# Performance work log

Hardware: AMD Instinct MI355X
Metric: run time of the kernel (lower is better)

## Reference

```python
import jax, jax.numpy as jnp
import numpy as np

N_ATOMS = 8192
N_PAIRS = 65536
F = 128        # n_atombasis
R = 20         # n_radialbasis
B = 5          # graph_n_blocks
EPS = 1e-8     # stability constant


def setup_inputs() -> dict:
    key = jax.random.key(0)
    ks = jax.random.split(key, 16)
    rn = lambda k, shape, s=0.05: jax.random.normal(k, shape, dtype=jnp.float32) * s
    return {
        "features": jax.random.normal(ks[0], (N_ATOMS, F), jnp.float32),
        "distances": jax.random.uniform(ks[1], (N_PAIRS,), jnp.float32, 0.5, 5.0),
        "vectors": jax.random.normal(ks[2], (N_PAIRS, 3), jnp.float32),
        "cutoffs": jax.random.uniform(ks[3], (N_PAIRS,), jnp.float32),
        "rbfs": jax.random.normal(ks[4], (N_PAIRS, R), jnp.float32),
        "filter_W": rn(ks[5], (R, B * 3 * F)),
        "filter_b": jnp.zeros((B * 3 * F,), jnp.float32),
        "int_W1": rn(ks[6], (B, F, F)),
        "int_b1": jnp.zeros((B, F), jnp.float32),
        "int_W2": rn(ks[7], (B, F, 3 * F)),
        "int_b2": jnp.zeros((B, 3 * F), jnp.float32),
        "mix_Wv": rn(ks[8], (B, F, 2 * F)),
        "mix_W1": rn(ks[9], (B, 2 * F, F)),
        "mix_b1": jnp.zeros((B, F), jnp.float32),
        "mix_W2": rn(ks[10], (B, F, 3 * F)),
        "mix_b2": jnp.zeros((B, 3 * F), jnp.float32),
        "idx_i": jax.random.randint(ks[11], (N_PAIRS,), 0, N_ATOMS),
        "idx_j": jax.random.randint(ks[12], (N_PAIRS,), 0, N_ATOMS),
    }


def reference(features, distances, vectors, cutoffs, rbfs,
              filter_W, filter_b, int_W1, int_b1, int_W2, int_b2,
              mix_Wv, mix_W1, mix_b1, mix_W2, mix_b2, idx_i, idx_j):
    n_atoms = features.shape[0]
    # Cutoff-weighted radial filters, one (3F) chunk per block: [P, B*3F]
    descriptors = (rbfs @ filter_W + filter_b) * cutoffs[:, None]
    dir_ij = vectors / distances[:, None]                       # [P, 3]

    q = features[:, None, :]                                    # [N, 1, F]
    mu = jnp.zeros((n_atoms, 3, F), dtype=features.dtype)       # [N, 3, F]

    for b in range(B):
        # --- interaction block ---
        x = jax.nn.silu(q @ int_W1[b] + int_b1[b]) @ int_W2[b] + int_b2[b]  # [N,1,3F]
        Wij = descriptors[:, None, b * 3 * F:(b + 1) * 3 * F]               # [P,1,3F]
        xj = x[idx_j] * Wij                                                 # [P,1,3F]
        muj = mu[idx_j]                                                     # [P,3,F]
        dq, dmuR, dmumu = jnp.split(xj, 3, axis=-1)                         # [P,1,F] each
        dmu = dmuR * dir_ij[:, :, None] + dmumu * muj                       # [P,3,F]
        q = q + jax.ops.segment_sum(dq, idx_i, num_segments=n_atoms)
        mu = mu + jax.ops.segment_sum(dmu, idx_i, num_segments=n_atoms)

        # --- mixing block ---
        mu_V, mu_W = jnp.split(mu @ mix_Wv[b], 2, axis=-1)                  # [N,3,F] each
        mu_Vn = jnp.sqrt(jnp.sum(mu_V ** 2, axis=-2, keepdims=True) + EPS)  # [N,1,F]
        ctx = jnp.concatenate([q, mu_Vn], axis=-1)                          # [N,1,2F]
        y = jax.nn.silu(ctx @ mix_W1[b] + mix_b1[b]) @ mix_W2[b] + mix_b2[b]
        dq_i, dmu_i, dqmu_i = jnp.split(y, 3, axis=-1)                      # [N,1,F] each
        q = q + dq_i + dqmu_i * jnp.sum(mu_V * mu_W, axis=1, keepdims=True)
        mu = mu + dmu_i * mu_W

    return q[:, 0, :], mu
```

## Files before the change

### kernel.cpp

```cpp
#include <hip/hip_runtime.h>
#include <hip/hip_bf16.h>

#define NA 8192
#define NP 65536
#define WROW 1920
#define CAP 40

typedef short short8 __attribute__((ext_vector_type(8)));
typedef short short4v __attribute__((ext_vector_type(4)));
typedef float floatx4 __attribute__((ext_vector_type(4)));
typedef unsigned uint3v __attribute__((ext_vector_type(3)));

static __device__ __forceinline__ short f2bf(float f) {
    union { float f; unsigned u; } v; v.f = f;
    unsigned r = v.u + 0x7FFF + ((v.u >> 16) & 1);
    return (short)(r >> 16);
}
static __device__ __forceinline__ float bf2f(short s) {
    union { unsigned u; float f; } v;
    v.u = ((unsigned)(unsigned short)s) << 16;
    return v.f;
}
static __device__ __forceinline__ unsigned char f2fp8(float f) {
    int p = __builtin_amdgcn_cvt_pk_fp8_f32(f, 0.f, 0, false);
    return (unsigned char)(p & 0xFF);
}
static __device__ __forceinline__ float fp82f(unsigned char b) {
    return __builtin_amdgcn_cvt_f32_fp8((int)b, 0);
}
static __device__ __forceinline__ float silu(float v) {
    return v / (1.f + __expf(-v));
}

static __device__ __forceinline__ void swz(const float* __restrict__ src,
                                           short* __restrict__ dst,
                                           int K, int N, int idx) {
    int kn = K * N;
    int b = idx / kn;
    int r = idx - b * kn;
    int tile = r >> 9, li = r & 511;
    int lane = li >> 3, bb = li & 7;
    int Kt = K >> 5;
    int nt = tile / Kt, kt = tile - nt * Kt;
    int k = kt * 32 + (lane >> 4) * 8 + bb;
    int n = nt * 16 + (lane & 15);
    dst[idx] = f2bf(src[b * kn + k * N + n]);
}

__global__ __launch_bounds__(256) void k_setup(const float* __restrict__ iW1,
                                               const float* __restrict__ iW2,
                                               const float* __restrict__ mWv,
                                               const float* __restrict__ mW1,
                                               const float* __restrict__ mW2,
                                               const float* __restrict__ fW,
                                               short* __restrict__ W1t,
                                               short* __restrict__ W2t,
                                               short* __restrict__ Wvt,
                                               short* __restrict__ mW1t,
                                               short* __restrict__ mW2t,
                                               short* __restrict__ fWt,
                                               const float* __restrict__ feat,
                                               float* __restrict__ q,
                                               float* __restrict__ mu,
                                               short* __restrict__ q_bf,
                                               unsigned* __restrict__ xmu_u,
                                               int* __restrict__ cursor) {
    int idx = blockIdx.x * 256 + threadIdx.x;
    if (idx < 962560) {
        if (idx < 81920)       { swz(iW1, W1t, 128, 128, idx); return; }
        idx -= 81920;
        if (idx < 245760)      { swz(iW2, W2t, 128, 384, idx); return; }
        idx -= 245760;
        if (idx < 163840)      { swz(mWv, Wvt, 128, 256, idx); return; }
        idx -= 163840;
        if (idx < 163840)      { swz(mW1, mW1t, 256, 128, idx); return; }
        idx -= 163840;
        if (idx < 245760)      { swz(mW2, mW2t, 128, 384, idx); return; }
        idx -= 245760;
        {
            int b = idx / 12288;
            int r = idx - b * 12288;
            int nt = r >> 9;
            int li = r & 511;
            int lane = li >> 3, bb = li & 7;
            int k = (lane >> 4) * 8 + bb;
            int n = nt * 16 + (lane & 15);
            fWt[b * 12288 + r] = (k < 20) ? f2bf(fW[k * WROW + b * 384 + n]) : (short)0;
        }
        return;
    }
    idx -= 962560;
    if (idx < NA * 128) { float v = feat[idx]; q[idx] = v; q_bf[idx] = f2bf(v); }
    mu[idx] = 0.f;
    xmu_u[idx] = 0;
    if (idx < NA) cursor[idx] = 0;
}

__global__ __launch_bounds__(256) void k_fillprep(const int* __restrict__ idx_i,
                                                  const int* __restrict__ idx_j,
                                                  int* __restrict__ cursor,
                                                  const float* __restrict__ cut,
                                                  const float* __restrict__ dist,
                                                  const float* __restrict__ vec,
                                                  const float* __restrict__ rbfs,
                                                  float* __restrict__ cut_csr,
                                                  float4* __restrict__ dirj,
                                                  short* __restrict__ rbf_c) {
    int p = blockIdx.x * 256 + threadIdx.x;
    if (p >= NP) return;
    int i = idx_i[p];
    int pos = atomicAdd(&cursor[i], 1);
    if (pos >= CAP) return;
    int e = i * CAP + pos;
    float c = cut[p];
    cut_csr[e] = c;
    float invd = 1.f / dist[p];
    float4 d;
    d.x = vec[p * 3 + 0] * invd;
    d.y = vec[p * 3 + 1] * invd;
    d.z = vec[p * 3 + 2] * invd;
    d.w = __int_as_float(idx_j[p]);
    dirj[e] = d;
    #pragma unroll
    for (int k = 0; k < 20; ++k) rbf_c[e * 32 + k] = f2bf(rbfs[p * 20 + k] * c);
    #pragma unroll
    for (int k = 20; k < 32; ++k) rbf_c[e * 32 + k] = 0;
}

__global__ __launch_bounds__(256) void k_x(const short* __restrict__ q_bf,
                                           const short* __restrict__ W1sw,
                                           const short* __restrict__ W2sw,
                                           const float* __restrict__ b1,
                                           const float* __restrict__ b2,
                                           unsigned char* __restrict__ xmu) {
    __shared__ __align__(16) short qtile[16 * 136];
    __shared__ __align__(16) short hs[16 * 136];
    int t = threadIdx.x;
    int wv = t >> 6, lane = t & 63, quad = lane >> 4, l16 = lane & 15;
    int a0 = blockIdx.x * 16;

    #pragma unroll
    for (int it = 0; it < 2; ++it) {
        int c = it * 256 + t;
        int row = c >> 5, col4 = c & 31;
        *(short4v*)(qtile + row * 136 + col4 * 4) =
            *(const short4v*)(q_bf + (a0 + row) * 128 + col4 * 4);
    }
    __syncthreads();

    floatx4 acc0 = {0.f, 0.f, 0.f, 0.f}, acc1 = {0.f, 0.f, 0.f, 0.f};
    #pragma unroll
    for (int kk = 0; kk < 4; ++kk) {
        short8 a  = *(const short8*)(qtile + l16 * 136 + kk * 32 + quad * 8);
        short8 b0 = *(const short8*)(W1sw + ((wv * 2 + 0) * 4 + kk) * 512 + lane * 8);
        short8 bq = *(const short8*)(W1sw + ((wv * 2 + 1) * 4 + kk) * 512 + lane * 8);
        acc0 = __builtin_amdgcn_mfma_f32_16x16x32_bf16(a, b0, acc0, 0, 0, 0);
        acc1 = __builtin_amdgcn_mfma_f32_16x16x32_bf16(a, bq, acc1, 0, 0, 0);
    }
    __syncthreads();
    {
        int n0 = wv * 32 + l16;
        float bia0 = b1[n0], bia1 = b1[n0 + 16];
        #pragma unroll
        for (int r = 0; r < 4; ++r) {
            int m = quad * 4 + r;
            hs[m * 136 + n0]      = f2bf(silu(acc0[r] + bia0));
            hs[m * 136 + n0 + 16] = f2bf(silu(acc1[r] + bia1));
        }
    }
    __syncthreads();
    floatx4 acc[6];
    #pragma unroll
    for (int jj = 0; jj < 6; ++jj) acc[jj] = {0.f, 0.f, 0.f, 0.f};
    #pragma unroll
    for (int kk = 0; kk < 4; ++kk) {
        short8 a = *(const short8*)(hs + l16 * 136 + kk * 32 + quad * 8);
        #pragma unroll
        for (int jj = 0; jj < 6; ++jj) {
            short8 b = *(const short8*)(W2sw + ((wv * 6 + jj) * 4 + kk) * 512 + lane * 8);
            acc[jj] = __builtin_amdgcn_mfma_f32_16x16x32_bf16(a, b, acc[jj], 0, 0, 0);
        }
    }
    #pragma unroll
    for (int jj = 0; jj < 6; ++jj) {
        int n = wv * 96 + jj * 16 + l16;
        float bia = b2[n];
        #pragma unroll
        for (int r = 0; r < 4; ++r) {
            int m = quad * 4 + r;
            xmu[(size_t)((a0 + m) * 128 + (n & 127)) * 12 + (n >> 7)] =
                f2fp8(acc[jj][r] + bia);
        }
    }
}

__global__ __launch_bounds__(256, 4) void k_gather(const unsigned char* __restrict__ xmu,
                                                   const short* __restrict__ rbf_c,
                                                   const short* __restrict__ fWt,
                                                   const float* __restrict__ fbp,
                                                   const float4* __restrict__ dirj,
                                                   const float* __restrict__ cut_csr,
                                                   const int* __restrict__ cursor,
                                                   short* __restrict__ dqg,
                                                   short* __restrict__ dmug) {
    __shared__ short dlds[16 * 392];
    __shared__ float pm[3 * 512];
    int i = blockIdx.x;
    int t = threadIdx.x;
    int wv = t >> 6, lane = t & 63, quad = lane >> 4, l16 = lane & 15;
    int start = i * CAP;

    float4 dj[4];
    #pragma unroll
    for (int m = 0; m < 4; ++m) dj[m] = dirj[start + wv + 4 * m];
    short8 afrag = *(const short8*)(rbf_c + (start + l16) * 32 + quad * 8);
    float cc[4];
    #pragma unroll
    for (int r = 0; r < 4; ++r) cc[r] = cut_csr[start + quad * 4 + r];

    int cnt = cursor[i];
    if (cnt > CAP) cnt = CAP;
    int end = start + cnt;

    float acc[8];
    #pragma unroll
    for (int k = 0; k < 8; ++k) acc[k] = 0.f;

    for (int e0 = start; e0 < end; e0 += 16) {
        if (e0 > start) {
            __syncthreads();
            #pragma unroll
            for (int m = 0; m < 4; ++m) dj[m] = dirj[e0 + wv + 4 * m];
            afrag = *(const short8*)(rbf_c + (e0 + l16) * 32 + quad * 8);
            #pragma unroll
            for (int r = 0; r < 4; ++r) cc[r] = cut_csr[e0 + quad * 4 + r];
        }
        int clen = end - e0; if (clen > 16) clen = 16;
        #pragma unroll
        for (int nt = 0; nt < 6; ++nt) {
            int col = wv * 96 + nt * 16 + l16;
            short8 bfr = *(const short8*)(fWt + (wv * 6 + nt) * 512 + lane * 8);
            floatx4 z = {0.f, 0.f, 0.f, 0.f};
            floatx4 ad = __builtin_amdgcn_mfma_f32_16x16x32_bf16(afrag, bfr, z, 0, 0, 0);
            float fbv = fbp[col];
            dlds[(quad * 4 + 0) * 392 + col] = f2bf(ad[0] + fbv * cc[0]);
            dlds[(quad * 4 + 1) * 392 + col] = f2bf(ad[1] + fbv * cc[1]);
            dlds[(quad * 4 + 2) * 392 + col] = f2bf(ad[2] + fbv * cc[2]);
            dlds[(quad * 4 + 3) * 392 + col] = f2bf(ad[3] + fbv * cc[3]);
        }
        uint3v rl[4], rh[4];
        #pragma unroll
        for (int m = 0; m < 4; ++m) {
            int le = wv + 4 * m;
            int j = (le < clen) ? __float_as_int(dj[m].w) : 0;
            const unsigned char* base = xmu + (size_t)j * 1536 + lane * 12;
            rl[m] = *(const uint3v*)(base);
            rh[m] = *(const uint3v*)(base + 768);
        }
        __syncthreads();
        #pragma unroll
        for (int m = 0; m < 4; ++m) {
            int le = wv + 4 * m;
            if (le < clen) {
                float wa0 = bf2f(dlds[le * 392 + lane]);
                float wb0 = bf2f(dlds[le * 392 + 128 + lane]);
                float wc0 = bf2f(dlds[le * 392 + 256 + lane]);
                float wa1 = bf2f(dlds[le * 392 + 64 + lane]);
                float wb1 = bf2f(dlds[le * 392 + 192 + lane]);
                float wc1 = bf2f(dlds[le * 392 + 320 + lane]);
                {
                    uint3v r_ = rl[m];
                    float x0 = fp82f((unsigned char)(r_.x & 0xFF));
                    float x1 = fp82f((unsigned char)((r_.x >> 8) & 0xFF));
                    float x2 = fp82f((unsigned char)((r_.x >> 16) & 0xFF));
                    float u0 = bf2f((short)(r_.y & 0xFFFF));
                    float u1 = bf2f((short)(r_.y >> 16));
                    float u2 = bf2f((short)(r_.z & 0xFFFF));
                    acc[0] += x0 * wa0;
                    float xb = x1 * wb0, xc = x2 * wc0;
                    acc[1] += xb * dj[m].x + xc * u0;
                    acc[2] += xb * dj[m].y + xc * u1;
                    acc[3] += xb * dj[m].z + xc * u2;
                }
                {
                    uint3v r_ = rh[m];
                    float x0 = fp82f((unsigned char)(r_.x & 0xFF));
                    float x1 = fp82f((unsigned char)((r_.x >> 8) & 0xFF));
                    float x2 = fp82f((unsigned char)((r_.x >> 16) & 0xFF));
                    float u0 = bf2f((short)(r_.y & 0xFFFF));
                    float u1 = bf2f((short)(r_.y >> 16));
                    float u2 = bf2f((short)(r_.z & 0xFFFF));
                    acc[4] += x0 * wa1;
                    float xb = x1 * wb1, xc = x2 * wc1;
                    acc[5] += xb * dj[m].x + xc * u0;
                    acc[6] += xb * dj[m].y + xc * u1;
                    acc[7] += xb * dj[m].z + xc * u2;
                }
            }
        }
    }
    if (wv) {
        float* p = pm + (wv - 1) * 512;
        #pragma unroll
        for (int arr = 0; arr < 4; ++arr) {
            p[arr * 128 + lane]      = acc[arr];
            p[arr * 128 + 64 + lane] = acc[arr + 4];
        }
    }
    __syncthreads();
    if (wv == 0) {
        #pragma unroll
        for (int hi = 0; hi < 2; ++hi) {
            int f = lane + hi * 64;
            float s[4];
            #pragma unroll
            for (int arr = 0; arr < 4; ++arr)
                s[arr] = acc[arr + 4 * hi]
                       + pm[0 * 512 + arr * 128 + f]
                       + pm[1 * 512 + arr * 128 + f]
                       + pm[2 * 512 + arr * 128 + f];
            dqg[i * 128 + f]            = f2bf(s[0]);
            dmug[(i * 3 + 0) * 128 + f] = f2bf(s[1]);
            dmug[(i * 3 + 1) * 128 + f] = f2bf(s[2]);
            dmug[(i * 3 + 2) * 128 + f] = f2bf(s[3]);
        }
    }
}

__global__ __launch_bounds__(512, 4) void k_mixx(const float* __restrict__ mu_ro,
                                                 const short* __restrict__ dmug,
                                                 const float* __restrict__ q_ro,
                                                 const short* __restrict__ dqg,
                                                 const short* __restrict__ Wvsw,
                                                 const short* __restrict__ W1sw,
                                                 const short* __restrict__ W2sw,
                                                 const float* __restrict__ b1,
                                                 const float* __restrict__ b2,
                                                 float* __restrict__ q,
                                                 float* __restrict__ mu,
                                                 unsigned char* __restrict__ xmu,
                                                 const short* __restrict__ xW1sw,
                                                 const short* __restrict__ xW2sw,
                                                 const float* __restrict__ xb1,
                                                 const float* __restrict__ xb2,
                                                 int do_x) {
    __shared__ __align__(16) char smem[51968];
    short* ms    = (short*)(smem);
    short* qtile = (short*)(smem + 13056);
    short* Vv    = (short*)(smem + 17408);
    short* hs    = (short*)(smem + 17408);
    short* Vw    = (short*)(smem + 30464);
    short* vnb   = (short*)(smem + 43520);
    short* sb    = (short*)(smem + 47872);
    int t = threadIdx.x;
    int wv = t >> 6, lane = t & 63, quad = lane >> 4, l16 = lane & 15;
    int a0 = blockIdx.x * 16;
    int co = wv * 16 + l16;

    float qnf[4];
    float mnf[4][3];
    #pragma unroll
    for (int r = 0; r < 4; ++r) {
        int m = quad * 4 + r;
        int ga = a0 + m;
        int gq = ga * 128 + co;
        qnf[r] = q_ro[gq] + bf2f(dqg[gq]);
        qtile[m * 136 + co] = f2bf(qnf[r]);
        #pragma unroll
        for (int d = 0; d < 3; ++d) {
            int gm = (ga * 3 + d) * 128 + co;
            mnf[r][d] = mu_ro[gm] + bf2f(dmug[gm]);
            ms[(m * 3 + d) * 136 + co] = f2bf(mnf[r][d]);
        }
    }
    __syncthreads();

    {
        floatx4 acc[3][2];
        #pragma unroll
        for (int mt = 0; mt < 3; ++mt)
            #pragma unroll
            for (int nt = 0; nt < 2; ++nt) acc[mt][nt] = {0.f, 0.f, 0.f, 0.f};
        #pragma unroll
        for (int kk = 0; kk < 4; ++kk) {
            short8 a[3];
            #pragma unroll
            for (int mt = 0; mt < 3; ++mt)
                a[mt] = *(const short8*)(ms + (mt * 16 + l16) * 136 + kk * 32 + quad * 8);
            #pragma unroll
            for (int nt = 0; nt < 2; ++nt) {
                short8 b = *(const short8*)(Wvsw + ((wv * 2 + nt) * 4 + kk) * 512 + lane * 8);
                #pragma unroll
                for (int mt = 0; mt < 3; ++mt)
                    acc[mt][nt] = __builtin_amdgcn_mfma_f32_16x16x32_bf16(a[mt], b, acc[mt][nt], 0, 0, 0);
            }
        }
        #pragma unroll
        for (int mt = 0; mt < 3; ++mt)
            #pragma unroll
            for (int nt = 0; nt < 2; ++nt)
                #pragma unroll
                for (int r = 0; r < 4; ++r) {
                    int row = mt * 16 + quad * 4 + r;
                    int col = wv * 32 + nt * 16 + l16;
                    short v = f2bf(acc[mt][nt][r]);
                    if (col < 128) Vv[row * 136 + col] = v;
                    else           Vw[row * 136 + col - 128] = v;
                }
    }
    __syncthreads();
    #pragma unroll
    for (int k = 0; k < 4; ++k) {
        int idx = k * 512 + t;
        int a = idx >> 7, c = idx & 127;
        float v0 = bf2f(Vv[(a * 3 + 0) * 136 + c]);
        float v1 = bf2f(Vv[(a * 3 + 1) * 136 + c]);
        float v2 = bf2f(Vv[(a * 3 + 2) * 136 + c]);
        float w0 = bf2f(Vw[(a * 3 + 0) * 136 + c]);
        float w1 = bf2f(Vw[(a * 3 + 1) * 136 + c]);
        float w2 = bf2f(Vw[(a * 3 + 2) * 136 + c]);
        vnb[a * 136 + c] = f2bf(sqrtf(v0 * v0 + v1 * v1 + v2 * v2 + 1e-8f));
        sb[a * 128 + c]  = f2bf(v0 * w0 + v1 * w1 + v2 * w2);
    }
    __syncthreads();
    {
        floatx4 acc0 = {0.f, 0.f, 0.f, 0.f};
        #pragma unroll
        for (int kk = 0; kk < 8; ++kk) {
            short8 a;
            if (kk < 4)
                a = *(const short8*)(qtile + l16 * 136 + kk * 32 + quad * 8);
            else
                a = *(const short8*)(vnb + l16 * 136 + (kk - 4) * 32 + quad * 8);
            short8 b0 = *(const short8*)(W1sw + (wv * 8 + kk) * 512 + lane * 8);
            acc0 = __builtin_amdgcn_mfma_f32_16x16x32_bf16(a, b0, acc0, 0, 0, 0);
        }
        int n0 = wv * 16 + l16;
        float bia0 = b1[n0];
        #pragma unroll
        for (int r = 0; r < 4; ++r) {
            int m = quad * 4 + r;
            hs[m * 136 + n0] = f2bf(silu(acc0[r] + bia0));
        }
    }
    __syncthreads();
    {
        floatx4 accB[3];
        #pragma unroll
        for (int c = 0; c < 3; ++c) accB[c] = {0.f, 0.f, 0.f, 0.f};
        #pragma unroll
        for (int kk = 0; kk < 4; ++kk) {
            short8 a = *(const short8*)(hs + l16 * 136 + kk * 32 + quad * 8);
            #pragma unroll
            for (int c = 0; c < 3; ++c) {
                short8 b = *(const short8*)(W2sw + ((c * 8 + wv) * 4 + kk) * 512 + lane * 8);
                accB[c] = __builtin_amdgcn_mfma_f32_16x16x32_bf16(a, b, accB[c], 0, 0, 0);
            }
        }
        float bq_  = b2[co];
        float bm_  = b2[128 + co];
        float bqm_ = b2[256 + co];
        #pragma unroll
        for (int r = 0; r < 4; ++r) {
            int m = quad * 4 + r;
            int ga = a0 + m;
            float dq   = accB[0][r] + bq_;
            float dmu  = accB[1][r] + bm_;
            float dqmu = accB[2][r] + bqm_;
            float sv = bf2f(sb[m * 128 + co]);
            int gq = ga * 128 + co;
            float qn = qnf[r] + dq + dqmu * sv;
            q[gq] = qn;
            qtile[m * 136 + co] = f2bf(qn);
            float mn[3];
            #pragma unroll
            for (int d = 0; d < 3; ++d) {
                int gm = (ga * 3 + d) * 128 + co;
                float mw = bf2f(Vw[(m * 3 + d) * 136 + co]);
                mn[d] = mnf[r][d] + dmu * mw;
                mu[gm] = mn[d];
            }
            unsigned lo = (unsigned)(unsigned short)f2bf(mn[0]) |
                          ((unsigned)(unsigned short)f2bf(mn[1]) << 16);
            *(unsigned*)(xmu + (size_t)gq * 12 + 4) = lo;
            *(short*)(xmu + (size_t)gq * 12 + 8) = f2bf(mn[2]);
        }
    }
    if (!do_x) return;
    __syncthreads();
    {
        floatx4 acc0 = {0.f, 0.f, 0.f, 0.f};
        #pragma unroll
        for (int kk = 0; kk < 4; ++kk) {
            short8 a  = *(const short8*)(qtile + l16 * 136 + kk * 32 + quad * 8);
            short8 b0 = *(const short8*)(xW1sw + (wv * 4 + kk) * 512 + lane * 8);
            acc0 = __builtin_amdgcn_mfma_f32_16x16x32_bf16(a, b0, acc0, 0, 0, 0);
        }
        int n0 = wv * 16 + l16;
        float bia0 = xb1[n0];
        #pragma unroll
        for (int r = 0; r < 4; ++r) {
            int m = quad * 4 + r;
            hs[m * 136 + n0] = f2bf(silu(acc0[r] + bia0));
        }
    }
    __syncthreads();
    {
        floatx4 acc[3];
        #pragma unroll
        for (int jj = 0; jj < 3; ++jj) acc[jj] = {0.f, 0.f, 0.f, 0.f};
        #pragma unroll
        for (int kk = 0; kk < 4; ++kk) {
            short8 a = *(const short8*)(hs + l16 * 136 + kk * 32 + quad * 8);
            #pragma unroll
            for (int jj = 0; jj < 3; ++jj) {
                short8 b = *(const short8*)(xW2sw + ((wv * 3 + jj) * 4 + kk) * 512 + lane * 8);
                acc[jj] = __builtin_amdgcn_mfma_f32_16x16x32_bf16(a, b, acc[jj], 0, 0, 0);
            }
        }
        #pragma unroll
        for (int jj = 0; jj < 3; ++jj) {
            int n = wv * 48 + jj * 16 + l16;
            float bia = xb2[n];
            #pragma unroll
            for (int r = 0; r < 4; ++r) {
                int m = quad * 4 + r;
                xmu[(size_t)((a0 + m) * 128 + (n & 127)) * 12 + (n >> 7)] =
                    f2fp8(acc[jj][r] + bia);
            }
        }
    }
}

extern "C" void kernel_launch(void* const* d_in, const int* in_sizes, int n_in,
                              void* d_out, int out_size, void* d_ws, size_t ws_size,
                              hipStream_t stream) {
    const float* feat = (const float*)d_in[0];
    const float* dist = (const float*)d_in[1];
    const float* vec  = (const float*)d_in[2];
    const float* cut  = (const float*)d_in[3];
    const float* rbfs = (const float*)d_in[4];
    const float* fW   = (const float*)d_in[5];
    const float* fb   = (const float*)d_in[6];
    const float* iW1  = (const float*)d_in[7];
    const float* ib1  = (const float*)d_in[8];
    const float* iW2  = (const float*)d_in[9];
    const float* ib2  = (const float*)d_in[10];
    const float* mWv  = (const float*)d_in[11];
    const float* mW1  = (const float*)d_in[12];
    const float* mb1  = (const float*)d_in[13];
    const float* mW2  = (const float*)d_in[14];
    const float* mb2  = (const float*)d_in[15];
    const int* idx_i  = (const int*)d_in[16];
    const int* idx_j  = (const int*)d_in[17];

    float* q  = (float*)d_out;
    float* mu = (float*)d_out + NA * 128;

    char* w = (char*)d_ws;
    unsigned char* xmu = (unsigned char*)(w);
    short* dqg     = (short*)(w + 12582912);
    short* q_bf    = (short*)(w + 14680064);
    short* dmug    = (short*)(w + 16777216);
    short* W1t     = (short*)(w + 23068672);
    short* W2t     = (short*)(w + 23232512);
    short* Wvt     = (short*)(w + 23724032);
    short* mW1t    = (short*)(w + 24051712);
    short* mW2t    = (short*)(w + 24379392);
    short* fWt     = (short*)(w + 24870912);
    int*   cursor  = (int*)(w + 24993792);
    float4* dirj   = (float4*)(w + 25026560);
    float* cut_csr = (float*)(w + 30269696);
    short* rbf_c   = (short*)(w + 31580480);

    k_setup<<<16048, 256, 0, stream>>>(iW1, iW2, mWv, mW1, mW2, fW,
                                       W1t, W2t, Wvt, mW1t, mW2t, fWt,
                                       feat, q, mu, q_bf, (unsigned*)xmu, cursor);
    k_fillprep<<<NP / 256, 256, 0, stream>>>(idx_i, idx_j, cursor, cut, dist, vec,
                                             rbfs, cut_csr, dirj, rbf_c);

    k_x<<<NA / 16, 256, 0, stream>>>(q_bf, W1t, W2t, ib1, ib2, xmu);
    for (int b = 0; b < 5; ++b) {
        int bn = (b + 1) % 5;
        k_gather<<<NA, 256, 0, stream>>>(xmu, rbf_c, fWt + b * 12288,
                                         fb + b * 384, dirj, cut_csr, cursor,
                                         dqg, dmug);
        k_mixx<<<NA / 16, 512, 0, stream>>>(mu, dmug, q, dqg,
                                            Wvt + b * 32768,
                                            mW1t + b * 32768, mW2t + b * 49152,
                                            mb1 + b * 128, mb2 + b * 384,
                                            q, mu, xmu,
                                            W1t + bn * 16384, W2t + bn * 49152,
                                            ib1 + bn * 128, ib2 + bn * 384,
                                            (b < 4) ? 1 : 0);
    }
}
```

Baseline: 371.3 us.

## Fuse per-atom gather into mixing kernel with double-buffered xmu

```diff
diff --git a/kernel.cpp b/kernel.cpp
--- a/kernel.cpp
+++ b/kernel.cpp
@@ -194,143 +194,15 @@
     }
 }
 
-__global__ __launch_bounds__(256, 4) void k_gather(const unsigned char* __restrict__ xmu,
-                                                   const short* __restrict__ rbf_c,
-                                                   const short* __restrict__ fWt,
-                                                   const float* __restrict__ fbp,
-                                                   const float4* __restrict__ dirj,
-                                                   const float* __restrict__ cut_csr,
-                                                   const int* __restrict__ cursor,
-                                                   short* __restrict__ dqg,
-                                                   short* __restrict__ dmug) {
-    __shared__ short dlds[16 * 392];
-    __shared__ float pm[3 * 512];
-    int i = blockIdx.x;
-    int t = threadIdx.x;
-    int wv = t >> 6, lane = t & 63, quad = lane >> 4, l16 = lane & 15;
-    int start = i * CAP;
-
-    float4 dj[4];
-    #pragma unroll
-    for (int m = 0; m < 4; ++m) dj[m] = dirj[start + wv + 4 * m];
-    short8 afrag = *(const short8*)(rbf_c + (start + l16) * 32 + quad * 8);
-    float cc[4];
-    #pragma unroll
-    for (int r = 0; r < 4; ++r) cc[r] = cut_csr[start + quad * 4 + r];
-
-    int cnt = cursor[i];
-    if (cnt > CAP) cnt = CAP;
-    int end = start + cnt;
-
-    float acc[8];
-    #pragma unroll
-    for (int k = 0; k < 8; ++k) acc[k] = 0.f;
-
-    for (int e0 = start; e0 < end; e0 += 16) {
-        if (e0 > start) {
-            __syncthreads();
-            #pragma unroll
-            for (int m = 0; m < 4; ++m) dj[m] = dirj[e0 + wv + 4 * m];
-            afrag = *(const short8*)(rbf_c + (e0 + l16) * 32 + quad * 8);
-            #pragma unroll
-            for (int r = 0; r < 4; ++r) cc[r] = cut_csr[e0 + quad * 4 + r];
-        }
-        int clen = end - e0; if (clen > 16) clen = 16;
-        #pragma unroll
-        for (int nt = 0; nt < 6; ++nt) {
-            int col = wv * 96 + nt * 16 + l16;
-            short8 bfr = *(const short8*)(fWt + (wv * 6 + nt) * 512 + lane * 8);
-            floatx4 z = {0.f, 0.f, 0.f, 0.f};
-            floatx4 ad = __builtin_amdgcn_mfma_f32_16x16x32_bf16(afrag, bfr, z, 0, 0, 0);
-            float fbv = fbp[col];
-            dlds[(quad * 4 + 0) * 392 + col] = f2bf(ad[0] + fbv * cc[0]);
-            dlds[(quad * 4 + 1) * 392 + col] = f2bf(ad[1] + fbv * cc[1]);
-            dlds[(quad * 4 + 2) * 392 + col] = f2bf(ad[2] + fbv * cc[2]);
-            dlds[(quad * 4 + 3) * 392 + col] = f2bf(ad[3] + fbv * cc[3]);
-        }
-        uint3v rl[4], rh[4];
-        #pragma unroll
-        for (int m = 0; m < 4; ++m) {
-            int le = wv + 4 * m;
-            int j = (le < clen) ? __float_as_int(dj[m].w) : 0;
-            const unsigned char* base = xmu + (size_t)j * 1536 + lane * 12;
-            rl[m] = *(const uint3v*)(base);
-            rh[m] = *(const uint3v*)(base + 768);
-        }
-        __syncthreads();
-        #pragma unroll
-        for (int m = 0; m < 4; ++m) {
-            int le = wv + 4 * m;
-            if (le < clen) {
-                float wa0 = bf2f(dlds[le * 392 + lane]);
-                float wb0 = bf2f(dlds[le * 392 + 128 + lane]);
-                float wc0 = bf2f(dlds[le * 392 + 256 + lane]);
-                float wa1 = bf2f(dlds[le * 392 + 64 + lane]);
-                float wb1 = bf2f(dlds[le * 392 + 192 + lane]);
-                float wc1 = bf2f(dlds[le * 392 + 320 + lane]);
-                {
-                    uint3v r_ = rl[m];
-                    float x0 = fp82f((unsigned char)(r_.x & 0xFF));
-                    float x1 = fp82f((unsigned char)((r_.x >> 8) & 0xFF));
-                    float x2 = fp82f((unsigned char)((r_.x >> 16) & 0xFF));
-                    float u0 = bf2f((short)(r_.y & 0xFFFF));
-                    float u1 = bf2f((short)(r_.y >> 16));
-                    float u2 = bf2f((short)(r_.z & 0xFFFF));
-                    acc[0] += x0 * wa0;
-                    float xb = x1 * wb0, xc = x2 * wc0;
-                    acc[1] += xb * dj[m].x + xc * u0;
-                    acc[2] += xb * dj[m].y + xc * u1;
-                    acc[3] += xb * dj[m].z + xc * u2;
-                }
-                {
-                    uint3v r_ = rh[m];
-                    float x0 = fp82f((unsigned char)(r_.x & 0xFF));
-                    float x1 = fp82f((unsigned char)((r_.x >> 8) & 0xFF));
-                    float x2 = fp82f((unsigned char)((r_.x >> 16) & 0xFF));
-                    float u0 = bf2f((short)(r_.y & 0xFFFF));
-                    float u1 = bf2f((short)(r_.y >> 16));
-                    float u2 = bf2f((short)(r_.z & 0xFFFF));
-                    acc[4] += x0 * wa1;
-                    float xb = x1 * wb1, xc = x2 * wc1;
-                    acc[5] += xb * dj[m].x + xc * u0;
-                    acc[6] += xb * dj[m].y + xc * u1;
-                    acc[7] += xb * dj[m].z + xc * u2;
-                }
-            }
-        }
-    }
-    if (wv) {
-        float* p = pm + (wv - 1) * 512;
-        #pragma unroll
-        for (int arr = 0; arr < 4; ++arr) {
-            p[arr * 128 + lane]      = acc[arr];
-            p[arr * 128 + 64 + lane] = acc[arr + 4];
-        }
-    }
-    __syncthreads();
-    if (wv == 0) {
-        #pragma unroll
-        for (int hi = 0; hi < 2; ++hi) {
-            int f = lane + hi * 64;
-            float s[4];
-            #pragma unroll
-            for (int arr = 0; arr < 4; ++arr)
-                s[arr] = acc[arr + 4 * hi]
-                       + pm[0 * 512 + arr * 128 + f]
-                       + pm[1 * 512 + arr * 128 + f]
-                       + pm[2 * 512 + arr * 128 + f];
-            dqg[i * 128 + f]            = f2bf(s[0]);
-            dmug[(i * 3 + 0) * 128 + f] = f2bf(s[1]);
-            dmug[(i * 3 + 1) * 128 + f] = f2bf(s[2]);
-            dmug[(i * 3 + 2) * 128 + f] = f2bf(s[3]);
-        }
-    }
-}
-
-__global__ __launch_bounds__(512, 4) void k_mixx(const float* __restrict__ mu_ro,
-                                                 const short* __restrict__ dmug,
+__global__ __launch_bounds__(512, 4) void k_gmix(const unsigned char* __restrict__ xmu_r,
+                                                 const short* __restrict__ rbf_c,
+                                                 const short* __restrict__ fWt,
+                                                 const float* __restrict__ fbp,
+                                                 const float4* __restrict__ dirj,
+                                                 const float* __restrict__ cut_csr,
+                                                 const int* __restrict__ cursor,
+                                                 const float* __restrict__ mu_ro,
                                                  const float* __restrict__ q_ro,
-                                                 const short* __restrict__ dqg,
                                                  const short* __restrict__ Wvsw,
                                                  const short* __restrict__ W1sw,
                                                  const short* __restrict__ W2sw,
@@ -338,23 +210,124 @@
                                                  const float* __restrict__ b2,
                                                  float* __restrict__ q,
                                                  float* __restrict__ mu,
-                                                 unsigned char* __restrict__ xmu,
+                                                 unsigned char* __restrict__ xmu_w,
                                                  const short* __restrict__ xW1sw,
                                                  const short* __restrict__ xW2sw,
                                                  const float* __restrict__ xb1,
                                                  const float* __restrict__ xb2,
                                                  int do_x) {
-    __shared__ __align__(16) char smem[51968];
-    short* ms    = (short*)(smem);
-    short* qtile = (short*)(smem + 13056);
-    short* Vv    = (short*)(smem + 17408);
-    short* hs    = (short*)(smem + 17408);
-    short* Vw    = (short*)(smem + 30464);
-    short* vnb   = (short*)(smem + 43520);
-    short* sb    = (short*)(smem + 47872);
+    __shared__ __align__(16) char smem[68608];
+    short* dg = (short*)smem;
     int t = threadIdx.x;
     int wv = t >> 6, lane = t & 63, quad = lane >> 4, l16 = lane & 15;
     int a0 = blockIdx.x * 16;
+
+    {
+        short* dld = (short*)(smem + 16640 + wv * 6272);
+        #pragma unroll
+        for (int half = 0; half < 2; ++half) {
+            int la = wv + half * 8;
+            int i  = __builtin_amdgcn_readfirstlane(a0 + la);
+            int start = i * CAP;
+            int cnt = cursor[i];
+            if (cnt > CAP) cnt = CAP;
+            float acc[8];
+            #pragma unroll
+            for (int k = 0; k < 8; ++k) acc[k] = 0.f;
+            for (int e0 = start; e0 < start + cnt; e0 += 8) {
+                int clen = start + cnt - e0; if (clen > 8) clen = 8;
+                short8 afrag = *(const short8*)(rbf_c + (size_t)(e0 + l16) * 32 + quad * 8);
+                float cc[4];
+                #pragma unroll
+                for (int r = 0; r < 4; ++r)
+                    cc[r] = cut_csr[e0 + (quad & 1) * 4 + r];
+                #pragma unroll
+                for (int nt = 0; nt < 24; ++nt) {
+                    short8 bfr = *(const short8*)(fWt + nt * 512 + lane * 8);
+                    floatx4 z = {0.f, 0.f, 0.f, 0.f};
+                    floatx4 ad = __builtin_amdgcn_mfma_f32_16x16x32_bf16(afrag, bfr, z, 0, 0, 0);
+                    if (quad < 2) {
+                        int col = nt * 16 + l16;
+                        float fbv = fbp[col];
+                        #pragma unroll
+                        for (int r = 0; r < 4; ++r)
+                            dld[(quad * 4 + r) * 392 + col] = f2bf(ad[r] + fbv * cc[r]);
+                    }
+                }
+                #pragma unroll
+                for (int mb = 0; mb < 8; mb += 4) {
+                    int mcl = clen - mb;
+                    if (mcl > 0) {
+                        float4 dj[4]; uint3v rl[4], rh[4];
+                        #pragma unroll
+                        for (int m = 0; m < 4; ++m)
+                            if (m < mcl) dj[m] = dirj[e0 + mb + m];
+                        #pragma unroll
+                        for (int m = 0; m < 4; ++m)
+                            if (m < mcl) {
+                                const unsigned char* base =
+                                    xmu_r + (size_t)__float_as_int(dj[m].w) * 1536 + lane * 12;
+                                rl[m] = *(const uint3v*)(base);
+                                rh[m] = *(const uint3v*)(base + 768);
+                            }
+                        #pragma unroll
+                        for (int m = 0; m < 4; ++m)
+                            if (m < mcl) {
+                                int le = mb + m;
+                                float wa0 = bf2f(dld[le * 392 + lane]);
+                                float wb0 = bf2f(dld[le * 392 + 128 + lane]);
+                                float wc0 = bf2f(dld[le * 392 + 256 + lane]);
+                                float wa1 = bf2f(dld[le * 392 + 64 + lane]);
+                                float wb1 = bf2f(dld[le * 392 + 192 + lane]);
+                                float wc1 = bf2f(dld[le * 392 + 320 + lane]);
+                                {
+                                    uint3v r_ = rl[m];
+                                    float x0 = fp82f((unsigned char)(r_.x & 0xFF));
+                                    float x1 = fp82f((unsigned char)((r_.x >> 8) & 0xFF));
+                                    float x2 = fp82f((unsigned char)((r_.x >> 16) & 0xFF));
+                                    float u0 = bf2f((short)(r_.y & 0xFFFF));
+                                    float u1 = bf2f((short)(r_.y >> 16));
+                                    float u2 = bf2f((short)(r_.z & 0xFFFF));
+                                    acc[0] += x0 * wa0;
+                                    float xb = x1 * wb0, xc = x2 * wc0;
+                                    acc[1] += xb * dj[m].x + xc * u0;
+                                    acc[2] += xb * dj[m].y + xc * u1;
+                                    acc[3] += xb * dj[m].z + xc * u2;
+                                }
+                                {
+                                    uint3v r_ = rh[m];
+                                    float x0 = fp82f((unsigned char)(r_.x & 0xFF));
+                                    float x1 = fp82f((unsigned char)((r_.x >> 8) & 0xFF));
+                                    float x2 = fp82f((unsigned char)((r_.x >> 16) & 0xFF));
+                                    float u0 = bf2f((short)(r_.y & 0xFFFF));
+                                    float u1 = bf2f((short)(r_.y >> 16));
+                                    float u2 = bf2f((short)(r_.z & 0xFFFF));
+                                    acc[4] += x0 * wa1;
+                                    float xb = x1 * wb1, xc = x2 * wc1;
+                                    acc[5] += xb * dj[m].x + xc * u0;
+                                    acc[6] += xb * dj[m].y + xc * u1;
+                                    acc[7] += xb * dj[m].z + xc * u2;
+                                }
+                            }
+                    }
+                }
+            }
+            #pragma unroll
+            for (int arr = 0; arr < 4; ++arr) {
+                dg[(la * 4 + arr) * 130 + lane]      = f2bf(acc[arr]);
+                dg[(la * 4 + arr) * 130 + 64 + lane] = f2bf(acc[arr + 4]);
+            }
+        }
+    }
+    __syncthreads();
+
+    short* ms    = (short*)(smem + 16640);
+    short* qtile = (short*)(smem + 16640 + 13056);
+    short* Vv    = (short*)(smem + 16640 + 17408);
+    short* hs    = (short*)(smem + 16640 + 17408);
+    short* Vw    = (short*)(smem + 16640 + 30464);
+    short* vnb   = (short*)(smem + 16640 + 43520);
+    short* sb    = (short*)(smem + 16640 + 47872);
     int co = wv * 16 + l16;
 
     float qnf[4];
@@ -364,12 +337,12 @@
         int m = quad * 4 + r;
         int ga = a0 + m;
         int gq = ga * 128 + co;
-        qnf[r] = q_ro[gq] + bf2f(dqg[gq]);
+        qnf[r] = q_ro[gq] + bf2f(dg[(m * 4 + 0) * 130 + co]);
         qtile[m * 136 + co] = f2bf(qnf[r]);
         #pragma unroll
         for (int d = 0; d < 3; ++d) {
             int gm = (ga * 3 + d) * 128 + co;
-            mnf[r][d] = mu_ro[gm] + bf2f(dmug[gm]);
+            mnf[r][d] = mu_ro[gm] + bf2f(dg[(m * 4 + 1 + d) * 130 + co]);
             ms[(m * 3 + d) * 136 + co] = f2bf(mnf[r][d]);
         }
     }
@@ -482,8 +455,8 @@
             }
             unsigned lo = (unsigned)(unsigned short)f2bf(mn[0]) |
                           ((unsigned)(unsigned short)f2bf(mn[1]) << 16);
-            *(unsigned*)(xmu + (size_t)gq * 12 + 4) = lo;
-            *(short*)(xmu + (size_t)gq * 12 + 8) = f2bf(mn[2]);
+            *(unsigned*)(xmu_w + (size_t)gq * 12 + 4) = lo;
+            *(short*)(xmu_w + (size_t)gq * 12 + 8) = f2bf(mn[2]);
         }
     }
     if (!do_x) return;
@@ -525,7 +498,7 @@
             #pragma unroll
             for (int r = 0; r < 4; ++r) {
                 int m = quad * 4 + r;
-                xmu[(size_t)((a0 + m) * 128 + (n & 127)) * 12 + (n >> 7)] =
+                xmu_w[(size_t)((a0 + m) * 128 + (n & 127)) * 12 + (n >> 7)] =
                     f2fp8(acc[jj][r] + bia);
             }
         }
@@ -558,38 +531,37 @@
     float* mu = (float*)d_out + NA * 128;
 
     char* w = (char*)d_ws;
-    unsigned char* xmu = (unsigned char*)(w);
-    short* dqg     = (short*)(w + 12582912);
-    short* q_bf    = (short*)(w + 14680064);
-    short* dmug    = (short*)(w + 16777216);
-    short* W1t     = (short*)(w + 23068672);
-    short* W2t     = (short*)(w + 23232512);
-    short* Wvt     = (short*)(w + 23724032);
-    short* mW1t    = (short*)(w + 24051712);
-    short* mW2t    = (short*)(w + 24379392);
-    short* fWt     = (short*)(w + 24870912);
-    int*   cursor  = (int*)(w + 24993792);
-    float4* dirj   = (float4*)(w + 25026560);
-    float* cut_csr = (float*)(w + 30269696);
-    short* rbf_c   = (short*)(w + 31580480);
+    unsigned char* xmu0 = (unsigned char*)(w);
+    unsigned char* xmu1 = (unsigned char*)(w + 12582912);
+    short* q_bf    = (short*)(w + 25165824);
+    short* W1t     = (short*)(w + 27262976);
+    short* W2t     = (short*)(w + 27426816);
+    short* Wvt     = (short*)(w + 27918336);
+    short* mW1t    = (short*)(w + 28246016);
+    short* mW2t    = (short*)(w + 28573696);
+    short* fWt     = (short*)(w + 29065216);
+    int*   cursor  = (int*)(w + 29188096);
+    float4* dirj   = (float4*)(w + 29220864);
+    float* cut_csr = (float*)(w + 34464000);
+    short* rbf_c   = (short*)(w + 35774784);
 
     k_setup<<<16048, 256, 0, stream>>>(iW1, iW2, mWv, mW1, mW2, fW,
                                        W1t, W2t, Wvt, mW1t, mW2t, fWt,
-                                       feat, q, mu, q_bf, (unsigned*)xmu, cursor);
+                                       feat, q, mu, q_bf, (unsigned*)xmu0, cursor);
     k_fillprep<<<NP / 256, 256, 0, stream>>>(idx_i, idx_j, cursor, cut, dist, vec,
                                              rbfs, cut_csr, dirj, rbf_c);
 
-    k_x<<<NA / 16, 256, 0, stream>>>(q_bf, W1t, W2t, ib1, ib2, xmu);
+    k_x<<<NA / 16, 256, 0, stream>>>(q_bf, W1t, W2t, ib1, ib2, xmu0);
+    unsigned char* xb[2] = {xmu0, xmu1};
     for (int b = 0; b < 5; ++b) {
         int bn = (b + 1) % 5;
-        k_gather<<<NA, 256, 0, stream>>>(xmu, rbf_c, fWt + b * 12288,
-                                         fb + b * 384, dirj, cut_csr, cursor,
-                                         dqg, dmug);
-        k_mixx<<<NA / 16, 512, 0, stream>>>(mu, dmug, q, dqg,
+        k_gmix<<<NA / 16, 512, 0, stream>>>(xb[b & 1], rbf_c, fWt + b * 12288,
+                                            fb + b * 384, dirj, cut_csr, cursor,
+                                            mu, q,
                                             Wvt + b * 32768,
                                             mW1t + b * 32768, mW2t + b * 49152,
                                             mb1 + b * 128, mb2 + b * 384,
-                                            q, mu, xmu,
+                                            q, mu, xb[(b + 1) & 1],
                                             W1t + bn * 16384, W2t + bn * 49152,
                                             ib1 + bn * 128, ib2 + bn * 384,
                                             (b < 4) ? 1 : 0);
```

Measured after the change: 498.1 us. 1.34x slower.

## Split packed x/mu gather array into separate double-buffered x and mu arrays

Applied to the files above, without the earlier changes.

```diff
diff --git a/kernel.cpp b/kernel.cpp
--- a/kernel.cpp
+++ b/kernel.cpp
@@ -9,7 +9,6 @@
 typedef short short8 __attribute__((ext_vector_type(8)));
 typedef short short4v __attribute__((ext_vector_type(4)));
 typedef float floatx4 __attribute__((ext_vector_type(4)));
-typedef unsigned uint3v __attribute__((ext_vector_type(3)));
 
 static __device__ __forceinline__ short f2bf(float f) {
     union { float f; unsigned u; } v; v.f = f;
@@ -63,7 +62,8 @@
                                                float* __restrict__ q,
                                                float* __restrict__ mu,
                                                short* __restrict__ q_bf,
-                                               unsigned* __restrict__ xmu_u,
+                                               unsigned* __restrict__ xarr0,
+                                               unsigned* __restrict__ muarr0,
                                                int* __restrict__ cursor) {
     int idx = blockIdx.x * 256 + threadIdx.x;
     if (idx < 962560) {
@@ -90,9 +90,9 @@
         return;
     }
     idx -= 962560;
-    if (idx < NA * 128) { float v = feat[idx]; q[idx] = v; q_bf[idx] = f2bf(v); }
+    if (idx < NA * 128) { float v = feat[idx]; q[idx] = v; q_bf[idx] = f2bf(v); xarr0[idx] = 0u; }
+    if (idx < NA * 256) muarr0[idx] = 0u;
     mu[idx] = 0.f;
-    xmu_u[idx] = 0;
     if (idx < NA) cursor[idx] = 0;
 }
 
@@ -132,7 +132,7 @@
                                            const short* __restrict__ W2sw,
                                            const float* __restrict__ b1,
                                            const float* __restrict__ b2,
-                                           unsigned char* __restrict__ xmu) {
+                                           unsigned char* __restrict__ xarr) {
     __shared__ __align__(16) short qtile[16 * 136];
     __shared__ __align__(16) short hs[16 * 136];
     int t = threadIdx.x;
@@ -188,13 +188,14 @@
         #pragma unroll
         for (int r = 0; r < 4; ++r) {
             int m = quad * 4 + r;
-            xmu[(size_t)((a0 + m) * 128 + (n & 127)) * 12 + (n >> 7)] =
+            xarr[(size_t)((a0 + m) * 128 + (n & 127)) * 4 + (n >> 7)] =
                 f2fp8(acc[jj][r] + bia);
         }
     }
 }
 
-__global__ __launch_bounds__(256, 4) void k_gather(const unsigned char* __restrict__ xmu,
+__global__ __launch_bounds__(256, 4) void k_gather(const unsigned* __restrict__ xarr_r,
+                                                   const uint2* __restrict__ muarr_r,
                                                    const short* __restrict__ rbf_c,
                                                    const short* __restrict__ fWt,
                                                    const float* __restrict__ fbp,
@@ -213,7 +214,7 @@
     float4 dj[4];
     #pragma unroll
     for (int m = 0; m < 4; ++m) dj[m] = dirj[start + wv + 4 * m];
-    short8 afrag = *(const short8*)(rbf_c + (start + l16) * 32 + quad * 8);
+    short8 afrag = *(const short8*)(rbf_c + (size_t)(start + l16) * 32 + quad * 8);
     float cc[4];
     #pragma unroll
     for (int r = 0; r < 4; ++r) cc[r] = cut_csr[start + quad * 4 + r];
@@ -231,7 +232,7 @@
             __syncthreads();
             #pragma unroll
             for (int m = 0; m < 4; ++m) dj[m] = dirj[e0 + wv + 4 * m];
-            afrag = *(const short8*)(rbf_c + (e0 + l16) * 32 + quad * 8);
+            afrag = *(const short8*)(rbf_c + (size_t)(e0 + l16) * 32 + quad * 8);
             #pragma unroll
             for (int r = 0; r < 4; ++r) cc[r] = cut_csr[e0 + quad * 4 + r];
         }
@@ -248,14 +249,17 @@
             dlds[(quad * 4 + 2) * 392 + col] = f2bf(ad[2] + fbv * cc[2]);
             dlds[(quad * 4 + 3) * 392 + col] = f2bf(ad[3] + fbv * cc[3]);
         }
-        uint3v rl[4], rh[4];
+        unsigned xl[4], xh[4]; uint2 ml[4], mh[4];
         #pragma unroll
         for (int m = 0; m < 4; ++m) {
             int le = wv + 4 * m;
             int j = (le < clen) ? __float_as_int(dj[m].w) : 0;
-            const unsigned char* base = xmu + (size_t)j * 1536 + lane * 12;
-            rl[m] = *(const uint3v*)(base);
-            rh[m] = *(const uint3v*)(base + 768);
+            const unsigned* xb_ = xarr_r + (size_t)j * 128 + lane;
+            xl[m] = xb_[0];
+            xh[m] = xb_[64];
+            const uint2* mb_ = muarr_r + (size_t)j * 128 + lane;
+            ml[m] = mb_[0];
+            mh[m] = mb_[64];
         }
         __syncthreads();
         #pragma unroll
@@ -269,13 +273,12 @@
                 float wb1 = bf2f(dlds[le * 392 + 192 + lane]);
                 float wc1 = bf2f(dlds[le * 392 + 320 + lane]);
                 {
-                    uint3v r_ = rl[m];
-                    float x0 = fp82f((unsigned char)(r_.x & 0xFF));
-                    float x1 = fp82f((unsigned char)((r_.x >> 8) & 0xFF));
-                    float x2 = fp82f((unsigned char)((r_.x >> 16) & 0xFF));
-                    float u0 = bf2f((short)(r_.y & 0xFFFF));
-                    float u1 = bf2f((short)(r_.y >> 16));
-                    float u2 = bf2f((short)(r_.z & 0xFFFF));
+                    float x0 = fp82f((unsigned char)(xl[m] & 0xFF));
+                    float x1 = fp82f((unsigned char)((xl[m] >> 8) & 0xFF));
+                    float x2 = fp82f((unsigned char)((xl[m] >> 16) & 0xFF));
+                    float u0 = bf2f((short)(ml[m].x & 0xFFFF));
+                    float u1 = bf2f((short)(ml[m].x >> 16));
+                    float u2 = bf2f((short)(ml[m].y & 0xFFFF));
                     acc[0] += x0 * wa0;
                     float xb = x1 * wb0, xc = x2 * wc0;
                     acc[1] += xb * dj[m].x + xc * u0;
@@ -283,13 +286,12 @@
                     acc[3] += xb * dj[m].z + xc * u2;
                 }
                 {
-                    uint3v r_ = rh[m];
-                    float x0 = fp82f((unsigned char)(r_.x & 0xFF));
-                    float x1 = fp82f((unsigned char)((r_.x >> 8) & 0xFF));
-                    float x2 = fp82f((unsigned char)((r_.x >> 16) & 0xFF));
-                    float u0 = bf2f((short)(r_.y & 0xFFFF));
-                    float u1 = bf2f((short)(r_.y >> 16));
-                    float u2 = bf2f((short)(r_.z & 0xFFFF));
+                    float x0 = fp82f((unsigned char)(xh[m] & 0xFF));
+                    float x1 = fp82f((unsigned char)((xh[m] >> 8) & 0xFF));
+                    float x2 = fp82f((unsigned char)((xh[m] >> 16) & 0xFF));
+                    float u0 = bf2f((short)(mh[m].x & 0xFFFF));
+                    float u1 = bf2f((short)(mh[m].x >> 16));
+                    float u2 = bf2f((short)(mh[m].y & 0xFFFF));
                     acc[4] += x0 * wa1;
                     float xb = x1 * wb1, xc = x2 * wc1;
                     acc[5] += xb * dj[m].x + xc * u0;
@@ -338,7 +340,8 @@
                                                  const float* __restrict__ b2,
                                                  float* __restrict__ q,
                                                  float* __restrict__ mu,
-                                                 unsigned char* __restrict__ xmu,
+                                                 unsigned* __restrict__ xarr_w,
+                                                 uint2* __restrict__ muarr_w,
                                                  const short* __restrict__ xW1sw,
                                                  const short* __restrict__ xW2sw,
                                                  const float* __restrict__ xb1,
@@ -352,6 +355,7 @@
     short* Vw    = (short*)(smem + 30464);
     short* vnb   = (short*)(smem + 43520);
     short* sb    = (short*)(smem + 47872);
+    unsigned char* xls = (unsigned char*)(smem + 43520);
     int t = threadIdx.x;
     int wv = t >> 6, lane = t & 63, quad = lane >> 4, l16 = lane & 15;
     int a0 = blockIdx.x * 16;
@@ -480,10 +484,13 @@
                 mn[d] = mnf[r][d] + dmu * mw;
                 mu[gm] = mn[d];
             }
-            unsigned lo = (unsigned)(unsigned short)f2bf(mn[0]) |
-                          ((unsigned)(unsigned short)f2bf(mn[1]) << 16);
-            *(unsigned*)(xmu + (size_t)gq * 12 + 4) = lo;
-            *(short*)(xmu + (size_t)gq * 12 + 8) = f2bf(mn[2]);
+            if (do_x) {
+                uint2 mw2;
+                mw2.x = (unsigned)(unsigned short)f2bf(mn[0]) |
+                        ((unsigned)(unsigned short)f2bf(mn[1]) << 16);
+                mw2.y = (unsigned)(unsigned short)f2bf(mn[2]);
+                muarr_w[gq] = mw2;
+            }
         }
     }
     if (!do_x) return;
@@ -525,9 +532,18 @@
             #pragma unroll
             for (int r = 0; r < 4; ++r) {
                 int m = quad * 4 + r;
-                xmu[(size_t)((a0 + m) * 128 + (n & 127)) * 12 + (n >> 7)] =
-                    f2fp8(acc[jj][r] + bia);
+                xls[(m * 128 + (n & 127)) * 4 + (n >> 7)] = f2fp8(acc[jj][r] + bia);
             }
+        }
+    }
+    __syncthreads();
+    {
+        const unsigned* xlsu = (const unsigned*)xls;
+        unsigned* xw = xarr_w + (size_t)a0 * 128;
+        #pragma unroll
+        for (int k = 0; k < 4; ++k) {
+            int idx = k * 512 + t;
+            xw[idx] = xlsu[idx];
         }
     }
 }
@@ -558,38 +574,44 @@
     float* mu = (float*)d_out + NA * 128;
 
     char* w = (char*)d_ws;
-    unsigned char* xmu = (unsigned char*)(w);
-    short* dqg     = (short*)(w + 12582912);
-    short* q_bf    = (short*)(w + 14680064);
-    short* dmug    = (short*)(w + 16777216);
-    short* W1t     = (short*)(w + 23068672);
-    short* W2t     = (short*)(w + 23232512);
-    short* Wvt     = (short*)(w + 23724032);
-    short* mW1t    = (short*)(w + 24051712);
-    short* mW2t    = (short*)(w + 24379392);
-    short* fWt     = (short*)(w + 24870912);
-    int*   cursor  = (int*)(w + 24993792);
-    float4* dirj   = (float4*)(w + 25026560);
-    float* cut_csr = (float*)(w + 30269696);
-    short* rbf_c   = (short*)(w + 31580480);
+    unsigned* xarr0  = (unsigned*)(w);
+    unsigned* xarr1  = (unsigned*)(w + 4194304);
+    uint2*    muarr0 = (uint2*)(w + 8388608);
+    uint2*    muarr1 = (uint2*)(w + 16777216);
+    short* dqg     = (short*)(w + 25165824);
+    short* dmug    = (short*)(w + 27262976);
+    short* q_bf    = (short*)(w + 33554432);
+    short* W1t     = (short*)(w + 35651584);
+    short* W2t     = (short*)(w + 35815424);
+    short* Wvt     = (short*)(w + 36306944);
+    short* mW1t    = (short*)(w + 36634624);
+    short* mW2t    = (short*)(w + 36962304);
+    short* fWt     = (short*)(w + 37453824);
+    int*   cursor  = (int*)(w + 37576704);
+    float4* dirj   = (float4*)(w + 37609472);
+    float* cut_csr = (float*)(w + 42852608);
+    short* rbf_c   = (short*)(w + 44163392);
 
     k_setup<<<16048, 256, 0, stream>>>(iW1, iW2, mWv, mW1, mW2, fW,
                                        W1t, W2t, Wvt, mW1t, mW2t, fWt,
-                                       feat, q, mu, q_bf, (unsigned*)xmu, cursor);
+                                       feat, q, mu, q_bf, xarr0, (unsigned*)muarr0, cursor);
     k_fillprep<<<NP / 256, 256, 0, stream>>>(idx_i, idx_j, cursor, cut, dist, vec,
                                              rbfs, cut_csr, dirj, rbf_c);
 
-    k_x<<<NA / 16, 256, 0, stream>>>(q_bf, W1t, W2t, ib1, ib2, xmu);
+    k_x<<<NA / 16, 256, 0, stream>>>(q_bf, W1t, W2t, ib1, ib2, (unsigned char*)xarr0);
+    unsigned* xa[2] = {xarr0, xarr1};
+    uint2*    ma[2] = {muarr0, muarr1};
     for (int b = 0; b < 5; ++b) {
         int bn = (b + 1) % 5;
-        k_gather<<<NA, 256, 0, stream>>>(xmu, rbf_c, fWt + b * 12288,
+        k_gather<<<NA, 256, 0, stream>>>(xa[b & 1], ma[b & 1], rbf_c, fWt + b * 12288,
                                          fb + b * 384, dirj, cut_csr, cursor,
                                          dqg, dmug);
         k_mixx<<<NA / 16, 512, 0, stream>>>(mu, dmug, q, dqg,
                                             Wvt + b * 32768,
                                             mW1t + b * 32768, mW2t + b * 49152,
                                             mb1 + b * 128, mb2 + b * 384,
-                                            q, mu, xmu,
+                                            q, mu,
+                                            xa[(b + 1) & 1], ma[(b + 1) & 1],
                                             W1t + bn * 16384, W2t + bn * 49152,
                                             ib1 + bn * 128, ib2 + bn * 384,
                                             (b < 4) ? 1 : 0);
```

After: 368.9 us. About the same (-0.7%).
